# Optimization experiments

Measured on AMD Instinct MI355X. Metric: run time of the kernel, lower is better.

## Reference

```python
import jax, jax.numpy as jnp
import numpy as np

N = 50000   # nodes per graph
E = 1600000 # edges per graph
F = 1024    # literal feature dim (hardcoded in source)
D = 256     # gcn_dims
B = 16384   # ent_ids batch
NUM_HOPS = 3
SLOPE = 0.01  # nn.LeakyReLU default


def spmm(row, col, val, X):
    # sparse [N,N] @ X[N,F] via COO gather + segment-sum
    return jax.ops.segment_sum(val[:, None] * X[col], row, num_segments=N)


def gcn(row, col, val, X, W, b):
    return jax.nn.leaky_relu(spmm(row, col, val, X) @ W + b, SLOPE)


def setup_inputs() -> dict:
    key = jax.random.key(0)
    ks = jax.random.split(key, 24)
    d = {}
    d['ent_lit'] = jax.random.normal(ks[0], (N, F), jnp.float32)
    d['rel_lit'] = jax.random.normal(ks[1], (N, F), jnp.float32)
    d['attr_lit'] = jax.random.normal(ks[2], (N, F), jnp.float32)
    d['ent_val'] = jax.random.uniform(ks[3], (E,), jnp.float32)
    d['rel_val'] = jax.random.uniform(ks[4], (E,), jnp.float32)
    d['attr_val'] = jax.random.uniform(ks[5], (E,), jnp.float32)
    s_in = 1.0 / np.sqrt(F)
    s_d = 1.0 / np.sqrt(D)
    d['W_ent'] = jax.random.normal(ks[6], (F, D), jnp.float32) * s_in
    d['b_ent'] = jnp.zeros((D,), jnp.float32)
    d['W_rel'] = jax.random.normal(ks[7], (F, D), jnp.float32) * s_in
    d['b_rel'] = jnp.zeros((D,), jnp.float32)
    d['W_attr'] = jax.random.normal(ks[8], (F, D), jnp.float32) * s_in
    d['b_attr'] = jnp.zeros((D,), jnp.float32)
    d['W_x'] = jax.random.normal(ks[9], (D, D), jnp.float32) * s_d
    d['b_x'] = jnp.zeros((D,), jnp.float32)
    d['W_lit'] = jax.random.normal(ks[10], (F, D), jnp.float32) * s_in
    d['b_lit'] = jnp.zeros((D,), jnp.float32)
    d['W_gate'] = jax.random.normal(ks[11], (D, D), jnp.float32) * s_d
    d['b_gate'] = jnp.zeros((D,), jnp.float32)
    d['ent_row'] = jax.random.randint(ks[12], (E,), 0, N, jnp.int32)
    d['ent_col'] = jax.random.randint(ks[13], (E,), 0, N, jnp.int32)
    d['rel_row'] = jax.random.randint(ks[14], (E,), 0, N, jnp.int32)
    d['rel_col'] = jax.random.randint(ks[15], (E,), 0, N, jnp.int32)
    d['attr_row'] = jax.random.randint(ks[16], (E,), 0, N, jnp.int32)
    d['attr_col'] = jax.random.randint(ks[17], (E,), 0, N, jnp.int32)
    d['ent_ids'] = jax.random.randint(ks[18], (B,), 0, N, jnp.int32)
    return d


def reference(ent_lit, rel_lit, attr_lit, ent_val, rel_val, attr_val,
              W_ent, b_ent, W_rel, b_rel, W_attr, b_attr, W_x, b_x,
              W_lit, b_lit, W_gate, b_gate,
              ent_row, ent_col, rel_row, rel_col, attr_row, attr_col, ent_ids):
    rel_repr = gcn(rel_row, rel_col, rel_val, rel_lit, W_rel, b_rel)[ent_ids]
    attr_repr = gcn(attr_row, attr_col, attr_val, attr_lit, W_attr, b_attr)[ent_ids]
    ent_literals = ent_lit[ent_ids] @ W_lit + b_lit
    # n-hop gated aggregation
    h = gcn(ent_row, ent_col, ent_val, ent_lit, W_ent, b_ent)
    for _ in range(1, NUM_HOPS):
        nxt = jax.nn.leaky_relu(spmm(ent_row, ent_col, ent_val, h) @ W_x + b_x, SLOPE)
        g = jax.nn.sigmoid(h @ W_gate + b_gate)
        h = g * nxt + (1.0 - g) * h
    ent_n_hop = h[ent_ids]
    return jnp.concatenate([ent_literals, ent_n_hop, rel_repr, attr_repr], axis=1)
```

## Files before the change

kernel.cpp:

```cpp
#include <hip/hip_runtime.h>
#include <math.h>

#define N_NODES 50000
#define N_EDGES 1600000
#define F_DIM 1024
#define D_DIM 256
#define B_IDS 16384

#define BROWS 1024
#define BKT 49
#define NB3 (3 * BKT)
#define CHUNK 4096

typedef __attribute__((ext_vector_type(8))) short bf16x8;
typedef __attribute__((ext_vector_type(4))) float f32x4;

static inline size_t alignup(size_t x) { return (x + 255) & ~(size_t)255; }

__device__ inline unsigned short f2bf(float f) {
  unsigned u = __float_as_uint(f);
  u += 0x7fffu + ((u >> 16) & 1u);
  return (unsigned short)(u >> 16);
}
__device__ inline float bf2f(unsigned short u) {
  return __uint_as_float(((unsigned)u) << 16);
}

__device__ inline void glds16(const void* g, void* l) {
  __builtin_amdgcn_global_load_lds(
      (const __attribute__((address_space(1))) void*)g,
      (__attribute__((address_space(3))) void*)l, 16, 0, 0);
}

struct TrArgs {
  const float* W[6];
  unsigned short* Wh[6];
  unsigned short* Wl[6];
  int K[6];
};

__global__ __launch_bounds__(256) void tr_all_k(TrArgs a) {
  const int z = blockIdx.z;
  const int K = a.K[z];
  if (blockIdx.x * 64 >= K) return;
  const float* W = a.W[z];
  unsigned short* Wt_hi = a.Wh[z];
  unsigned short* Wt_lo = a.Wl[z];
  __shared__ float t[64][65];
  const int k0 = blockIdx.x * 64, n0 = blockIdx.y * 64;
  const int tid = threadIdx.x;
  const int rr = tid >> 4, c4 = (tid & 15) * 4;
#pragma unroll
  for (int q = 0; q < 4; ++q) {
    int row = q * 16 + rr;
    const float4 v = *reinterpret_cast<const float4*>(W + (size_t)(k0 + row) * 256 + n0 + c4);
    t[row][c4 + 0] = v.x; t[row][c4 + 1] = v.y; t[row][c4 + 2] = v.z; t[row][c4 + 3] = v.w;
  }
  __syncthreads();
#pragma unroll
  for (int q = 0; q < 4; ++q) {
    int n = q * 16 + rr;
    ushort4 oh, ol;
    float w0 = t[c4 + 0][n], w1 = t[c4 + 1][n], w2 = t[c4 + 2][n], w3 = t[c4 + 3][n];
    oh.x = f2bf(w0); ol.x = f2bf(w0 - bf2f(oh.x));
    oh.y = f2bf(w1); ol.y = f2bf(w1 - bf2f(oh.y));
    oh.z = f2bf(w2); ol.z = f2bf(w2 - bf2f(oh.z));
    oh.w = f2bf(w3); ol.w = f2bf(w3 - bf2f(oh.w));
    *reinterpret_cast<ushort4*>(Wt_hi + (size_t)(n0 + n) * K + k0 + c4) = oh;
    *reinterpret_cast<ushort4*>(Wt_lo + (size_t)(n0 + n) * K + k0 + c4) = ol;
  }
}


__global__ __launch_bounds__(256) void bcount_k(
    const int* __restrict__ r0, const int* __restrict__ r1, const int* __restrict__ r2,
    int* __restrict__ bcnt)
{
  __shared__ int h[NB3];
  const int t = threadIdx.x;
  for (int i = t; i < NB3; i += 256) h[i] = 0;
  __syncthreads();
  const long long cbase = (long long)blockIdx.x * CHUNK;
  const long long tot = 3LL * N_EDGES;
#pragma unroll
  for (int j = 0; j < 16; ++j) {
    long long idx = cbase + j * 256 + t;
    if (idx < tot) {
      int g = (int)(idx / N_EDGES);
      int e = (int)(idx - (long long)g * N_EDGES);
      int row = (g == 0 ? r0 : g == 1 ? r1 : r2)[e];
      atomicAdd(&h[g * BKT + (row >> 10)], 1);
    }
  }
  __syncthreads();
  for (int i = t; i < NB3; i += 256)
    if (h[i]) atomicAdd(&bcnt[i], h[i]);
}

__global__ void bscan_k(const int* __restrict__ bcnt, int* __restrict__ flatBase,
                        int* __restrict__ cursor) {
  __shared__ int c[NB3];
  const int t = threadIdx.x;
  if (t < NB3) c[t] = bcnt[t];
  __syncthreads();
  if (t < 3) {
    int acc = t * N_EDGES;
    for (int b = 0; b < BKT; ++b) {
      int i = t * BKT + b;
      int v = c[i];
      flatBase[i] = acc;
      cursor[i] = acc;
      acc += v;
    }
  }
  if (t == 0) flatBase[NB3] = 3 * N_EDGES;
}

__global__ __launch_bounds__(256) void bpart_k(
    const int* __restrict__ r0, const int* __restrict__ c0, const float* __restrict__ v0,
    const int* __restrict__ r1, const int* __restrict__ c1, const float* __restrict__ v1,
    const int* __restrict__ r2, const int* __restrict__ c2, const float* __restrict__ v2,
    int* __restrict__ cursor, int2* __restrict__ packed)
{
  __shared__ int hs[256];
  __shared__ int ls[NB3];
  __shared__ int cur[NB3];
  __shared__ int clm[NB3];
  __shared__ int2 stg[CHUNK];
  __shared__ int tgt[CHUNK];
  const int t = threadIdx.x;
  const long long cbase = (long long)blockIdx.x * CHUNK;
  const long long tot = 3LL * N_EDGES;
  hs[t] = 0;
  __syncthreads();
  int rows_[16], gbs_[16];
#pragma unroll
  for (int j = 0; j < 16; ++j) {
    long long idx = cbase + j * 256 + t;
    int gb = -1, row = 0;
    if (idx < tot) {
      int g = (int)(idx / N_EDGES);
      int e = (int)(idx - (long long)g * N_EDGES);
      row = (g == 0 ? r0 : g == 1 ? r1 : r2)[e];
      gb = g * BKT + (row >> 10);
      atomicAdd(&hs[gb], 1);
    }
    gbs_[j] = gb; rows_[j] = row;
  }
  __syncthreads();
  const int myh = hs[t];
  if (t < NB3) clm[t] = atomicAdd(&cursor[t], myh);
  for (int off = 1; off < 256; off <<= 1) {
    int v = (t >= off) ? hs[t - off] : 0;
    __syncthreads();
    hs[t] += v;
    __syncthreads();
  }
  const int excl = hs[t] - myh;
  if (t < NB3) { ls[t] = excl; cur[t] = excl; }
  __syncthreads();
#pragma unroll
  for (int j = 0; j < 16; ++j) {
    const int gb = gbs_[j];
    if (gb >= 0) {
      long long idx = cbase + j * 256 + t;
      int g = (int)(idx / N_EDGES);
      int e = (int)(idx - (long long)g * N_EDGES);
      int col = (g == 0 ? c0 : g == 1 ? c1 : c2)[e];
      float vv = (g == 0 ? v0 : g == 1 ? v1 : v2)[e];
      int slot = atomicAdd(&cur[gb], 1);
      stg[slot] = make_int2(rows_[j] | (col << 16), __float_as_int(vv));
      tgt[slot] = clm[gb] + (slot - ls[gb]);
    }
  }
  __syncthreads();
  const int cnt = (int)min((long long)CHUNK, tot - cbase);
  for (int i = t; i < cnt; i += 256) packed[tgt[i]] = stg[i];
}

__global__ __launch_bounds__(256) void bfinal_k(
    const int2* __restrict__ packed, const int* __restrict__ flatBase,
    int* __restrict__ row_ptr3, int2* __restrict__ cv3)
{
  __shared__ int hist[BROWS];
  __shared__ int part[256];
  const int gb = blockIdx.x;
  const int g = gb / BKT, b = gb % BKT;
  const int rb = b * BROWS;
  const int nrows = min(BROWS, N_NODES - rb);
  const int base = flatBase[gb];
  const int cnt = flatBase[gb + 1] - base;
  const int cvb = base - g * N_EDGES;
  const int t = threadIdx.x;
  for (int i = t; i < BROWS; i += 256) hist[i] = 0;
  __syncthreads();
  for (int i = t; i < cnt; i += 256) {
    int rc = packed[base + i].x;
    atomicAdd(&hist[(rc & 0xffff) - rb], 1);
  }
  __syncthreads();
  const int l0 = hist[4 * t], l1 = hist[4 * t + 1], l2 = hist[4 * t + 2], l3 = hist[4 * t + 3];
  const int s = l0 + l1 + l2 + l3;
  part[t] = s;
  __syncthreads();
  for (int off = 1; off < 256; off <<= 1) {
    int v = (t >= off) ? part[t - off] : 0;
    __syncthreads();
    part[t] += v;
    __syncthreads();
  }
  const int pexcl = part[t] - s;
  const int e0 = pexcl, e1 = e0 + l0, e2 = e1 + l1, e3 = e2 + l2;
  hist[4 * t] = e0; hist[4 * t + 1] = e1; hist[4 * t + 2] = e2; hist[4 * t + 3] = e3;
  int* rp = row_ptr3 + (size_t)g * (N_NODES + 1);
  if (4 * t + 0 < nrows) rp[rb + 4 * t + 0] = cvb + e0;
  if (4 * t + 1 < nrows) rp[rb + 4 * t + 1] = cvb + e1;
  if (4 * t + 2 < nrows) rp[rb + 4 * t + 2] = cvb + e2;
  if (4 * t + 3 < nrows) rp[rb + 4 * t + 3] = cvb + e3;
  if (rb + BROWS >= N_NODES && t == 0) rp[N_NODES] = N_EDGES;
  __syncthreads();
  for (int i = t; i < cnt; i += 256) {
    int2 p = packed[base + i];
    int row = p.x & 0xffff;
    int col = ((unsigned)p.x) >> 16;
    int pos = atomicAdd(&hist[row - rb], 1);
    cv3[base + pos] = make_int2(col, p.y);
  }
}

__global__ void flag_k(const int* __restrict__ ids, unsigned char* __restrict__ flag, int B) {
  int i = blockIdx.x * blockDim.x + threadIdx.x;
  if (i < B) flag[ids[i]] = 1;
}

__global__ __launch_bounds__(256) void spmm_k(
    const int* __restrict__ row_ptr, const int2* __restrict__ cv,
    const unsigned short* __restrict__ srcb, float* __restrict__ dst,
    unsigned short* __restrict__ dstb,
    const float* __restrict__ bias, int do_leaky,
    const unsigned char* __restrict__ flag, int n)
{
  int r = (blockIdx.x << 2) + (threadIdx.x >> 6);
  if (r >= n) return;
  if (flag && !flag[r]) return;
  const int lane = threadIdx.x & 63;
  const int c0 = lane << 2;
  int e0 = row_ptr[r], e1 = row_ptr[r + 1];
  float a0 = 0.f, a1 = 0.f, a2 = 0.f, a3 = 0.f;
  int e = e0;
  for (; e + 3 < e1; e += 4) {
    int2 p0 = cv[e], p1 = cv[e + 1], p2 = cv[e + 2], p3 = cv[e + 3];
    const ushort4 x0 = *reinterpret_cast<const ushort4*>(srcb + (size_t)p0.x * D_DIM + c0);
    const ushort4 x1 = *reinterpret_cast<const ushort4*>(srcb + (size_t)p1.x * D_DIM + c0);
    const ushort4 x2 = *reinterpret_cast<const ushort4*>(srcb + (size_t)p2.x * D_DIM + c0);
    const ushort4 x3 = *reinterpret_cast<const ushort4*>(srcb + (size_t)p3.x * D_DIM + c0);
    const float v0 = __int_as_float(p0.y), v1 = __int_as_float(p1.y);
    const float v2 = __int_as_float(p2.y), v3 = __int_as_float(p3.y);
    a0 = fmaf(v0, bf2f(x0.x), a0); a1 = fmaf(v0, bf2f(x0.y), a1);
    a2 = fmaf(v0, bf2f(x0.z), a2); a3 = fmaf(v0, bf2f(x0.w), a3);
    a0 = fmaf(v1, bf2f(x1.x), a0); a1 = fmaf(v1, bf2f(x1.y), a1);
    a2 = fmaf(v1, bf2f(x1.z), a2); a3 = fmaf(v1, bf2f(x1.w), a3);
    a0 = fmaf(v2, bf2f(x2.x), a0); a1 = fmaf(v2, bf2f(x2.y), a1);
    a2 = fmaf(v2, bf2f(x2.z), a2); a3 = fmaf(v2, bf2f(x2.w), a3);
    a0 = fmaf(v3, bf2f(x3.x), a0); a1 = fmaf(v3, bf2f(x3.y), a1);
    a2 = fmaf(v3, bf2f(x3.z), a2); a3 = fmaf(v3, bf2f(x3.w), a3);
  }
  for (; e < e1; ++e) {
    int2 p = cv[e];
    float v = __int_as_float(p.y);
    const ushort4 x = *reinterpret_cast<const ushort4*>(srcb + (size_t)p.x * D_DIM + c0);
    a0 = fmaf(v, bf2f(x.x), a0); a1 = fmaf(v, bf2f(x.y), a1);
    a2 = fmaf(v, bf2f(x.z), a2); a3 = fmaf(v, bf2f(x.w), a3);
  }
  if (bias) {
    const float4 b = *reinterpret_cast<const float4*>(bias + c0);
    a0 += b.x; a1 += b.y; a2 += b.z; a3 += b.w;
  }
  if (do_leaky) {
    a0 = a0 > 0.f ? a0 : 0.01f * a0;
    a1 = a1 > 0.f ? a1 : 0.01f * a1;
    a2 = a2 > 0.f ? a2 : 0.01f * a2;
    a3 = a3 > 0.f ? a3 : 0.01f * a3;
  }
  *reinterpret_cast<float4*>(dst + (size_t)r * D_DIM + c0) =
      make_float4(a0, a1, a2, a3);
  if (dstb) {
    ushort4 o;
    o.x = f2bf(a0); o.y = f2bf(a1); o.z = f2bf(a2); o.w = f2bf(a3);
    *reinterpret_cast<ushort4*>(dstb + (size_t)r * D_DIM + c0) = o;
  }
}

template<int KT, int MODE>
__global__ __launch_bounds__(512, 4) void mm_k(
    const float* __restrict__ Aptr,
    const unsigned short* __restrict__ Wt_hi,
    const unsigned short* __restrict__ Wt_lo,
    const float* __restrict__ bias,
    float* __restrict__ C, int ldc, int ccol0, int M,
    const int* __restrict__ rowidx,
    const float* __restrict__ nxt, const float* __restrict__ hin,
    unsigned short* __restrict__ Cb)
{
  __shared__ __align__(16) unsigned char smem[32768];
  const int tid = threadIdx.x;
  const int wid = tid >> 6, lane = tid & 63;
  const int wm = wid & 3, wn = wid >> 2;
  const int bm = blockIdx.x * 128;
  const int l15 = lane & 15, lk = lane >> 4;

  int mrow[2];
  const float* arow[2];
#pragma unroll
  for (int mi = 0; mi < 2; ++mi) {
    int m = bm + wm * 32 + mi * 16 + l15;
    mrow[mi] = m;
    int sr = (m < M) ? (rowidx ? rowidx[m] : m) : 0;
    arow[mi] = Aptr + (size_t)sr * KT;
  }

  const int s1 = tid, s2 = tid + 512;
  const size_t go1 = (size_t)(s1 >> 2) * KT + ((((s1 & 3) - ((s1 >> 3) & 3)) & 3) << 3);
  const size_t go2 = (size_t)(s2 >> 2) * KT + ((((s2 & 3) - ((s2 >> 3) & 3)) & 3) << 3);

  f32x4 acc[2][8] = {};
  for (int kc = 0; kc < KT / 32; ++kc) {
    const int kk = kc * 32;
    __syncthreads();
    glds16(Wt_hi + go1 + kk, smem + s1 * 16);
    glds16(Wt_hi + go2 + kk, smem + s2 * 16);
    glds16(Wt_lo + go1 + kk, smem + 16384 + s1 * 16);
    glds16(Wt_lo + go2 + kk, smem + 16384 + s2 * 16);
    const int ka = kk + lk * 8;
    bf16x8 ah[2], al[2];
#pragma unroll
    for (int mi = 0; mi < 2; ++mi) {
      bf16x8 th = {0, 0, 0, 0, 0, 0, 0, 0};
      bf16x8 tl = {0, 0, 0, 0, 0, 0, 0, 0};
      if (mrow[mi] < M) {
        const float* p = arow[mi] + ka;
        const float4 x = *reinterpret_cast<const float4*>(p);
        const float4 y = *reinterpret_cast<const float4*>(p + 4);
#define SPLIT_A(i, val) { unsigned short h_ = f2bf(val); th[i] = (short)h_; \
                          tl[i] = (short)f2bf((val) - bf2f(h_)); }
        SPLIT_A(0, x.x) SPLIT_A(1, x.y) SPLIT_A(2, x.z) SPLIT_A(3, x.w)
        SPLIT_A(4, y.x) SPLIT_A(5, y.y) SPLIT_A(6, y.z) SPLIT_A(7, y.w)
#undef SPLIT_A
      }
      ah[mi] = th; al[mi] = tl;
    }
    __syncthreads();
#pragma unroll
    for (int f = 0; f < 8; ++f) {
      const int n = wn * 128 + f * 16 + l15;
      const int boff = n * 64 + (((lk + (l15 >> 1)) & 3) << 4);
      const bf16x8 bh = *reinterpret_cast<const bf16x8*>(smem + boff);
      const bf16x8 bl = *reinterpret_cast<const bf16x8*>(smem + 16384 + boff);
#pragma unroll
      for (int mi = 0; mi < 2; ++mi) {
        acc[mi][f] = __builtin_amdgcn_mfma_f32_16x16x32_bf16(ah[mi], bh, acc[mi][f], 0, 0, 0);
        acc[mi][f] = __builtin_amdgcn_mfma_f32_16x16x32_bf16(al[mi], bh, acc[mi][f], 0, 0, 0);
        acc[mi][f] = __builtin_amdgcn_mfma_f32_16x16x32_bf16(ah[mi], bl, acc[mi][f], 0, 0, 0);
      }
    }
  }

  __syncthreads();

#pragma unroll
  for (int mi = 0; mi < 2; ++mi) {
    const int rbase = bm + wm * 32 + mi * 16 + lk * 4;
    int hsrc[4];
    if (MODE == 2) {
#pragma unroll
      for (int r = 0; r < 4; ++r) {
        const int row = rbase + r;
        hsrc[r] = (rowidx && row < M) ? rowidx[row] : row;
      }
    }
#pragma unroll
    for (int f = 0; f < 8; ++f) {
      const int col = wn * 128 + f * 16 + l15;
      const float bc = bias ? bias[col] : 0.f;
#pragma unroll
      for (int r = 0; r < 4; ++r) {
        const int row = rbase + r;
        if (row >= M) continue;
        float v = acc[mi][f][r] + bc;
        if (MODE == 1) v = v > 0.f ? v : 0.01f * v;
        if (MODE == 2) {
          const float g = 1.f / (1.f + __expf(-v));
          const float nv = nxt[(size_t)row * D_DIM + col];
          const float hv = hin[(size_t)hsrc[r] * D_DIM + col];
          v = g * nv + (1.f - g) * hv;
        }
        C[(size_t)row * ldc + ccol0 + col] = v;
        if (Cb) Cb[(size_t)row * D_DIM + col] = f2bf(v);
      }
    }
  }
}

__global__ __launch_bounds__(256) void gather_k(const float* __restrict__ src,
                                                const int* __restrict__ ids,
                                                float* __restrict__ dst, int ccol0, int B)
{
  int i = (blockIdx.x << 2) + (threadIdx.x >> 6);
  if (i >= B) return;
  const int lane = threadIdx.x & 63;
  const int c0 = lane << 2;
  const float4 v = *reinterpret_cast<const float4*>(src + (size_t)ids[i] * D_DIM + c0);
  *reinterpret_cast<float4*>(dst + (size_t)i * 1024 + ccol0 + c0) = v;
}

extern "C" void kernel_launch(void* const* d_in, const int* in_sizes, int n_in,
                              void* d_out, int out_size, void* d_ws, size_t ws_size,
                              hipStream_t stream)
{
  const float* ent_lit = (const float*)d_in[0];
  const float* rel_lit = (const float*)d_in[1];
  const float* attr_lit = (const float*)d_in[2];
  const float* ent_val = (const float*)d_in[3];
  const float* rel_val = (const float*)d_in[4];
  const float* attr_val = (const float*)d_in[5];
  const float* W_ent = (const float*)d_in[6];
  const float* b_ent = (const float*)d_in[7];
  const float* W_rel = (const float*)d_in[8];
  const float* b_rel = (const float*)d_in[9];
  const float* W_attr = (const float*)d_in[10];
  const float* b_attr = (const float*)d_in[11];
  const float* W_x = (const float*)d_in[12];
  const float* b_x = (const float*)d_in[13];
  const float* W_lit = (const float*)d_in[14];
  const float* b_lit = (const float*)d_in[15];
  const float* W_gate = (const float*)d_in[16];
  const float* b_gate = (const float*)d_in[17];
  const int* ent_row = (const int*)d_in[18];
  const int* ent_col = (const int*)d_in[19];
  const int* rel_row = (const int*)d_in[20];
  const int* rel_col = (const int*)d_in[21];
  const int* attr_row = (const int*)d_in[22];
  const int* attr_col = (const int*)d_in[23];
  const int* ent_ids = (const int*)d_in[24];
  float* out = (float*)d_out;

  char* p = (char*)d_ws;
  const size_t bufsz = alignup((size_t)N_NODES * D_DIM * 4);
  const size_t bufszb = alignup((size_t)N_NODES * D_DIM * 2);
  const size_t wsz_f = alignup((size_t)F_DIM * D_DIM * 2);
  const size_t wsz_d = alignup((size_t)D_DIM * D_DIM * 2);
  float* B0 = (float*)p; p += bufsz;
  float* B1 = (float*)p; p += bufsz;
  unsigned short* B0b = (unsigned short*)p; p += bufszb;
  unsigned short* B1b = (unsigned short*)p; p += bufszb;
  float* P = (float*)B1b;
  unsigned short* Wh_ent = (unsigned short*)p; p += wsz_f;
  unsigned short* Wl_ent = (unsigned short*)p; p += wsz_f;
  unsigned short* Wh_rel = (unsigned short*)p; p += wsz_f;
  unsigned short* Wl_rel = (unsigned short*)p; p += wsz_f;
  unsigned short* Wh_attr = (unsigned short*)p; p += wsz_f;
  unsigned short* Wl_attr = (unsigned short*)p; p += wsz_f;
  unsigned short* Wh_lit = (unsigned short*)p; p += wsz_f;
  unsigned short* Wl_lit = (unsigned short*)p; p += wsz_f;
  unsigned short* Wh_x = (unsigned short*)p; p += wsz_d;
  unsigned short* Wl_x = (unsigned short*)p; p += wsz_d;
  unsigned short* Wh_gate = (unsigned short*)p; p += wsz_d;
  unsigned short* Wl_gate = (unsigned short*)p; p += wsz_d;
  int* row_ptr3 = (int*)p; p += alignup((size_t)3 * (N_NODES + 1) * 4);
  int* bcnt = (int*)p; p += alignup((size_t)NB3 * 4);
  int* flatBase = (int*)p; p += alignup((size_t)(NB3 + 1) * 4);
  int* cursor = (int*)p; p += alignup((size_t)NB3 * 4);
  unsigned char* flags = (unsigned char*)p; p += alignup((size_t)N_NODES);
  int2* cv3 = (int2*)p; p += alignup((size_t)3 * N_EDGES * 8);
  if ((size_t)(p - (char*)d_ws) > ws_size) return;

  int2* packed = (int2*)B0;

  const int* rp_ent = row_ptr3;
  const int* rp_rel = row_ptr3 + (N_NODES + 1);
  const int* rp_attr = row_ptr3 + 2 * (N_NODES + 1);
  const int2* cv_ent = cv3;
  const int2* cv_rel = cv3 + (size_t)N_EDGES;
  const int2* cv_attr = cv3 + (size_t)2 * N_EDGES;

  dim3 blk(256), blk512(512);
  const int nchunks = (int)((3LL * N_EDGES + CHUNK - 1) / CHUNK);
  dim3 g_spmm((N_NODES + 3) / 4);
  dim3 g_gather((B_IDS + 3) / 4);
  dim3 g_mm_big((N_NODES + 127) / 128);
  dim3 g_mm_ids(B_IDS / 128);

  TrArgs ta;
  ta.W[0] = W_ent;  ta.Wh[0] = Wh_ent;  ta.Wl[0] = Wl_ent;  ta.K[0] = F_DIM;
  ta.W[1] = W_rel;  ta.Wh[1] = Wh_rel;  ta.Wl[1] = Wl_rel;  ta.K[1] = F_DIM;
  ta.W[2] = W_attr; ta.Wh[2] = Wh_attr; ta.Wl[2] = Wl_attr; ta.K[2] = F_DIM;
  ta.W[3] = W_lit;  ta.Wh[3] = Wh_lit;  ta.Wl[3] = Wl_lit;  ta.K[3] = F_DIM;
  ta.W[4] = W_x;    ta.Wh[4] = Wh_x;    ta.Wl[4] = Wl_x;    ta.K[4] = D_DIM;
  ta.W[5] = W_gate; ta.Wh[5] = Wh_gate; ta.Wl[5] = Wl_gate; ta.K[5] = D_DIM;
  tr_all_k<<<dim3(F_DIM / 64, 4, 6), blk, 0, stream>>>(ta);

  hipMemsetAsync(bcnt, 0, NB3 * sizeof(int), stream);
  bcount_k<<<dim3(nchunks), blk, 0, stream>>>(ent_row, rel_row, attr_row, bcnt);
  bscan_k<<<dim3(1), blk, 0, stream>>>(bcnt, flatBase, cursor);
  bpart_k<<<dim3(nchunks), blk, 0, stream>>>(ent_row, ent_col, ent_val,
                                             rel_row, rel_col, rel_val,
                                             attr_row, attr_col, attr_val,
                                             cursor, packed);
  bfinal_k<<<dim3(NB3), blk, 0, stream>>>(packed, flatBase, row_ptr3, cv3);

  hipMemsetAsync(flags, 0, N_NODES, stream);
  flag_k<<<dim3(B_IDS / 256), blk, 0, stream>>>(ent_ids, flags, B_IDS);

  mm_k<F_DIM, 0><<<g_mm_big, blk512, 0, stream>>>(rel_lit, Wh_rel, Wl_rel, nullptr, B0, D_DIM, 0,
                                                  N_NODES, nullptr, nullptr, nullptr, B0b);
  spmm_k<<<g_spmm, blk, 0, stream>>>(rp_rel, cv_rel, B0b, B1, nullptr, b_rel, 1, flags, N_NODES);
  gather_k<<<g_gather, blk, 0, stream>>>(B1, ent_ids, out, 512, B_IDS);

  mm_k<F_DIM, 0><<<g_mm_big, blk512, 0, stream>>>(attr_lit, Wh_attr, Wl_attr, nullptr, B0, D_DIM, 0,
                                                  N_NODES, nullptr, nullptr, nullptr, B0b);
  spmm_k<<<g_spmm, blk, 0, stream>>>(rp_attr, cv_attr, B0b, B1, nullptr, b_attr, 1, flags, N_NODES);
  gather_k<<<g_gather, blk, 0, stream>>>(B1, ent_ids, out, 768, B_IDS);

  mm_k<F_DIM, 0><<<g_mm_ids, blk512, 0, stream>>>(ent_lit, Wh_lit, Wl_lit, b_lit, out, 1024, 0,
                                                  B_IDS, ent_ids, nullptr, nullptr, nullptr);

  mm_k<F_DIM, 0><<<g_mm_big, blk512, 0, stream>>>(ent_lit, Wh_ent, Wl_ent, nullptr, B0, D_DIM, 0,
                                                  N_NODES, nullptr, nullptr, nullptr, B0b);
  spmm_k<<<g_spmm, blk, 0, stream>>>(rp_ent, cv_ent, B0b, B1, B1b, b_ent, 1, nullptr, N_NODES);
  spmm_k<<<g_spmm, blk, 0, stream>>>(rp_ent, cv_ent, B1b, B0, nullptr, nullptr, 0, nullptr, N_NODES);
  mm_k<D_DIM, 1><<<g_mm_big, blk512, 0, stream>>>(B0, Wh_x, Wl_x, b_x, B0, D_DIM, 0,
                                                  N_NODES, nullptr, nullptr, nullptr, nullptr);
  mm_k<D_DIM, 2><<<g_mm_big, blk512, 0, stream>>>(B1, Wh_gate, Wl_gate, b_gate, B1, D_DIM, 0,
                                                  N_NODES, nullptr, B0, B1, B1b);
  spmm_k<<<g_spmm, blk, 0, stream>>>(rp_ent, cv_ent, B1b, B0, nullptr, nullptr, 0, flags, N_NODES);
  mm_k<D_DIM, 1><<<g_mm_ids, blk512, 0, stream>>>(B0, Wh_x, Wl_x, b_x, P, D_DIM, 0,
                                                  B_IDS, ent_ids, nullptr, nullptr, nullptr);
  mm_k<D_DIM, 2><<<g_mm_ids, blk512, 0, stream>>>(B1, Wh_gate, Wl_gate, b_gate, out, 1024, 256,
                                                  B_IDS, ent_ids, P, B1, nullptr);
}
```

Measured before the change: 1.302 ms.

## Retile dense GEMM into 64x128 blocks with 256 threads and 64-wide K steps

Adds a new mm_k variant that tiles output as 64 rows by 128 columns over a 2D grid, uses 256-thread blocks, and stages 64-wide K chunks of the split bf16 weights per barrier pair. This halves the number of K-loop synchronisations and raises the block count for better occupancy and load balance on the K=1024 projections. The old 128x256 kernel is kept as mmw_k for the in-place full-graph hop GEMMs, where the new tiling would let column tiles race with in-place writes. The trade-off is that each A row is now read and split to bf16 twice, once per column tile. The smem swizzle index is also changed from l15 to n.

```diff
diff --git a/kernel.cpp b/kernel.cpp
--- a/kernel.cpp
+++ b/kernel.cpp
@@ -292,7 +292,130 @@
 }
 
 template<int KT, int MODE>
-__global__ __launch_bounds__(512, 4) void mm_k(
+__global__ __launch_bounds__(256, 4) void mm_k(
+    const float* __restrict__ Aptr,
+    const unsigned short* __restrict__ Wt_hi,
+    const unsigned short* __restrict__ Wt_lo,
+    const float* __restrict__ bias,
+    float* __restrict__ C, int ldc, int ccol0, int M,
+    const int* __restrict__ rowidx,
+    const float* __restrict__ nxt, const float* __restrict__ hin,
+    unsigned short* __restrict__ Cb)
+{
+  __shared__ __align__(16) unsigned char smem[32768];
+  const int tid = threadIdx.x;
+  const int wid = tid >> 6, lane = tid & 63;
+  const int wm = wid & 1, wn = wid >> 1;
+  const int bm = blockIdx.y * 64;
+  const int bn0 = blockIdx.x * 128;
+  const int l15 = lane & 15, lk = lane >> 4;
+
+  int mrow[2];
+  const float* arow[2];
+#pragma unroll
+  for (int mi = 0; mi < 2; ++mi) {
+    int m = bm + wm * 32 + mi * 16 + l15;
+    mrow[mi] = m;
+    int sr = (m < M) ? (rowidx ? rowidx[m] : m) : 0;
+    arow[mi] = Aptr + (size_t)sr * KT;
+  }
+
+  const int st_n = tid >> 2;
+  const int st_seg = ((tid & 3) - ((tid >> 3) & 3)) & 3;
+  const size_t goA = (size_t)(bn0 + st_n) * KT + st_seg * 8;
+  const size_t goB = goA + (size_t)64 * KT;
+  const unsigned ldA = tid * 16, ldB = tid * 16 + 4096;
+
+  f32x4 acc[2][4] = {};
+  for (int kc = 0; kc < KT / 64; ++kc) {
+    const int kk = kc * 64;
+    __syncthreads();
+    glds16(Wt_hi + goA + kk,      smem + ldA);
+    glds16(Wt_hi + goB + kk,      smem + ldB);
+    glds16(Wt_hi + goA + kk + 32, smem + 8192 + ldA);
+    glds16(Wt_hi + goB + kk + 32, smem + 8192 + ldB);
+    glds16(Wt_lo + goA + kk,      smem + 16384 + ldA);
+    glds16(Wt_lo + goB + kk,      smem + 16384 + ldB);
+    glds16(Wt_lo + goA + kk + 32, smem + 24576 + ldA);
+    glds16(Wt_lo + goB + kk + 32, smem + 24576 + ldB);
+    bf16x8 ah[2][2], al[2][2];
+#pragma unroll
+    for (int ks = 0; ks < 2; ++ks) {
+      const int ka = kk + ks * 32 + lk * 8;
+#pragma unroll
+      for (int mi = 0; mi < 2; ++mi) {
+        bf16x8 th = {0, 0, 0, 0, 0, 0, 0, 0};
+        bf16x8 tl = {0, 0, 0, 0, 0, 0, 0, 0};
+        if (mrow[mi] < M) {
+          const float* p = arow[mi] + ka;
+          const float4 x = *reinterpret_cast<const float4*>(p);
+          const float4 y = *reinterpret_cast<const float4*>(p + 4);
+#define SPLIT_A(i, val) { unsigned short h_ = f2bf(val); th[i] = (short)h_; \
+                          tl[i] = (short)f2bf((val) - bf2f(h_)); }
+          SPLIT_A(0, x.x) SPLIT_A(1, x.y) SPLIT_A(2, x.z) SPLIT_A(3, x.w)
+          SPLIT_A(4, y.x) SPLIT_A(5, y.y) SPLIT_A(6, y.z) SPLIT_A(7, y.w)
+#undef SPLIT_A
+        }
+        ah[ks][mi] = th; al[ks][mi] = tl;
+      }
+    }
+    __syncthreads();
+#pragma unroll
+    for (int ks = 0; ks < 2; ++ks) {
+#pragma unroll
+      for (int f = 0; f < 4; ++f) {
+        const int n = wn * 64 + f * 16 + l15;
+        const int boff = ks * 8192 + n * 64 + (((lk + (n >> 1)) & 3) << 4);
+        const bf16x8 bh = *reinterpret_cast<const bf16x8*>(smem + boff);
+        const bf16x8 bl = *reinterpret_cast<const bf16x8*>(smem + 16384 + boff);
+#pragma unroll
+        for (int mi = 0; mi < 2; ++mi) {
+          acc[mi][f] = __builtin_amdgcn_mfma_f32_16x16x32_bf16(ah[ks][mi], bh, acc[mi][f], 0, 0, 0);
+          acc[mi][f] = __builtin_amdgcn_mfma_f32_16x16x32_bf16(al[ks][mi], bh, acc[mi][f], 0, 0, 0);
+          acc[mi][f] = __builtin_amdgcn_mfma_f32_16x16x32_bf16(ah[ks][mi], bl, acc[mi][f], 0, 0, 0);
+        }
+      }
+    }
+  }
+
+  __syncthreads();
+
+#pragma unroll
+  for (int mi = 0; mi < 2; ++mi) {
+    const int rbase = bm + wm * 32 + mi * 16 + lk * 4;
+    int hsrc[4];
+    if (MODE == 2) {
+#pragma unroll
+      for (int r = 0; r < 4; ++r) {
+        const int row = rbase + r;
+        hsrc[r] = (rowidx && row < M) ? rowidx[row] : row;
+      }
+    }
+#pragma unroll
+    for (int f = 0; f < 4; ++f) {
+      const int col = bn0 + wn * 64 + f * 16 + l15;
+      const float bc = bias ? bias[col] : 0.f;
+#pragma unroll
+      for (int r = 0; r < 4; ++r) {
+        const int row = rbase + r;
+        if (row >= M) continue;
+        float v = acc[mi][f][r] + bc;
+        if (MODE == 1) v = v > 0.f ? v : 0.01f * v;
+        if (MODE == 2) {
+          const float g = 1.f / (1.f + __expf(-v));
+          const float nv = nxt[(size_t)row * D_DIM + col];
+          const float hv = hin[(size_t)hsrc[r] * D_DIM + col];
+          v = g * nv + (1.f - g) * hv;
+        }
+        C[(size_t)row * ldc + ccol0 + col] = v;
+        if (Cb) Cb[(size_t)row * D_DIM + col] = f2bf(v);
+      }
+    }
+  }
+}
+
+template<int KT, int MODE>
+__global__ __launch_bounds__(512, 4) void mmw_k(
     const float* __restrict__ Aptr,
     const unsigned short* __restrict__ Wt_hi,
     const unsigned short* __restrict__ Wt_lo,
@@ -353,7 +476,7 @@
 #pragma unroll
     for (int f = 0; f < 8; ++f) {
       const int n = wn * 128 + f * 16 + l15;
-      const int boff = n * 64 + (((lk + (l15 >> 1)) & 3) << 4);
+      const int boff = n * 64 + (((lk + (n >> 1)) & 3) << 4);
       const bf16x8 bh = *reinterpret_cast<const bf16x8*>(smem + boff);
       const bf16x8 bl = *reinterpret_cast<const bf16x8*>(smem + 16384 + boff);
 #pragma unroll
@@ -487,8 +610,9 @@
   const int nchunks = (int)((3LL * N_EDGES + CHUNK - 1) / CHUNK);
   dim3 g_spmm((N_NODES + 3) / 4);
   dim3 g_gather((B_IDS + 3) / 4);
-  dim3 g_mm_big((N_NODES + 127) / 128);
-  dim3 g_mm_ids(B_IDS / 128);
+  dim3 g_mm_big(2, (N_NODES + 63) / 64);
+  dim3 g_mm_ids(2, B_IDS / 64);
+  dim3 g_mmw_big((N_NODES + 127) / 128);
 
   TrArgs ta;
   ta.W[0] = W_ent;  ta.Wh[0] = Wh_ent;  ta.Wl[0] = Wl_ent;  ta.K[0] = F_DIM;
@@ -511,30 +635,30 @@
   hipMemsetAsync(flags, 0, N_NODES, stream);
   flag_k<<<dim3(B_IDS / 256), blk, 0, stream>>>(ent_ids, flags, B_IDS);
 
-  mm_k<F_DIM, 0><<<g_mm_big, blk512, 0, stream>>>(rel_lit, Wh_rel, Wl_rel, nullptr, B0, D_DIM, 0,
-                                                  N_NODES, nullptr, nullptr, nullptr, B0b);
+  mm_k<F_DIM, 0><<<g_mm_big, blk, 0, stream>>>(rel_lit, Wh_rel, Wl_rel, nullptr, B0, D_DIM, 0,
+                                               N_NODES, nullptr, nullptr, nullptr, B0b);
   spmm_k<<<g_spmm, blk, 0, stream>>>(rp_rel, cv_rel, B0b, B1, nullptr, b_rel, 1, flags, N_NODES);
   gather_k<<<g_gather, blk, 0, stream>>>(B1, ent_ids, out, 512, B_IDS);
 
-  mm_k<F_DIM, 0><<<g_mm_big, blk512, 0, stream>>>(attr_lit, Wh_attr, Wl_attr, nullptr, B0, D_DIM, 0,
-                                                  N_NODES, nullptr, nullptr, nullptr, B0b);
+  mm_k<F_DIM, 0><<<g_mm_big, blk, 0, stream>>>(attr_lit, Wh_attr, Wl_attr, nullptr, B0, D_DIM, 0,
+                                               N_NODES, nullptr, nullptr, nullptr, B0b);
   spmm_k<<<g_spmm, blk, 0, stream>>>(rp_attr, cv_attr, B0b, B1, nullptr, b_attr, 1, flags, N_NODES);
   gather_k<<<g_gather, blk, 0, stream>>>(B1, ent_ids, out, 768, B_IDS);
 
-  mm_k<F_DIM, 0><<<g_mm_ids, blk512, 0, stream>>>(ent_lit, Wh_lit, Wl_lit, b_lit, out, 1024, 0,
-                                                  B_IDS, ent_ids, nullptr, nullptr, nullptr);
-
-  mm_k<F_DIM, 0><<<g_mm_big, blk512, 0, stream>>>(ent_lit, Wh_ent, Wl_ent, nullptr, B0, D_DIM, 0,
-                                                  N_NODES, nullptr, nullptr, nullptr, B0b);
+  mm_k<F_DIM, 0><<<g_mm_ids, blk, 0, stream>>>(ent_lit, Wh_lit, Wl_lit, b_lit, out, 1024, 0,
+                                               B_IDS, ent_ids, nullptr, nullptr, nullptr);
+
+  mm_k<F_DIM, 0><<<g_mm_big, blk, 0, stream>>>(ent_lit, Wh_ent, Wl_ent, nullptr, B0, D_DIM, 0,
+                                               N_NODES, nullptr, nullptr, nullptr, B0b);
   spmm_k<<<g_spmm, blk, 0, stream>>>(rp_ent, cv_ent, B0b, B1, B1b, b_ent, 1, nullptr, N_NODES);
   spmm_k<<<g_spmm, blk, 0, stream>>>(rp_ent, cv_ent, B1b, B0, nullptr, nullptr, 0, nullptr, N_NODES);
-  mm_k<D_DIM, 1><<<g_mm_big, blk512, 0, stream>>>(B0, Wh_x, Wl_x, b_x, B0, D_DIM, 0,
-                                                  N_NODES, nullptr, nullptr, nullptr, nullptr);
-  mm_k<D_DIM, 2><<<g_mm_big, blk512, 0, stream>>>(B1, Wh_gate, Wl_gate, b_gate, B1, D_DIM, 0,
-                                                  N_NODES, nullptr, B0, B1, B1b);
+  mmw_k<D_DIM, 1><<<g_mmw_big, blk512, 0, stream>>>(B0, Wh_x, Wl_x, b_x, B0, D_DIM, 0,
+                                                    N_NODES, nullptr, nullptr, nullptr, nullptr);
+  mmw_k<D_DIM, 2><<<g_mmw_big, blk512, 0, stream>>>(B1, Wh_gate, Wl_gate, b_gate, B1, D_DIM, 0,
+                                                    N_NODES, nullptr, B0, B1, B1b);
   spmm_k<<<g_spmm, blk, 0, stream>>>(rp_ent, cv_ent, B1b, B0, nullptr, nullptr, 0, flags, N_NODES);
-  mm_k<D_DIM, 1><<<g_mm_ids, blk512, 0, stream>>>(B0, Wh_x, Wl_x, b_x, P, D_DIM, 0,
-                                                  B_IDS, ent_ids, nullptr, nullptr, nullptr);
-  mm_k<D_DIM, 2><<<g_mm_ids, blk512, 0, stream>>>(B1, Wh_gate, Wl_gate, b_gate, out, 1024, 256,
-                                                  B_IDS, ent_ids, P, B1, nullptr);
-}
+  mm_k<D_DIM, 1><<<g_mm_ids, blk, 0, stream>>>(B0, Wh_x, Wl_x, b_x, P, D_DIM, 0,
+                                               B_IDS, ent_ids, nullptr, nullptr, nullptr);
+  mm_k<D_DIM, 2><<<g_mm_ids, blk, 0, stream>>>(B1, Wh_gate, Wl_gate, b_gate, out, 1024, 256,
+                                               B_IDS, ent_ids, P, B1, nullptr);
+}
```

New measurement: 1.419 ms. 1.09x slower.
